# Kernel tuning notes

Measured on AMD Instinct MI355X. Metric: run time of the kernel, lower is better.

Reference implementation:

```python
import jax, jax.numpy as jnp
import numpy as np

N, K, M = 4096, 128, 512  # conformers, dihedrals, atoms


def setup_inputs() -> dict:
    key = jax.random.key(0)
    k1, k2 = jax.random.split(key)
    inp = jax.random.normal(k1, (N, K), dtype=jnp.float32)          # target dihedral deltas (rad)
    pos0 = jax.random.normal(k2, (N, M, 3), dtype=jnp.float32)      # initial conformer coordinates
    base = jnp.arange(K, dtype=jnp.int32)
    # chain molecule: dihedral k defined by atoms (k, k+1, k+2, k+3)
    angles = jnp.stack([base, base + 1, base + 2, base + 3], axis=1)  # (K, 4)
    # rdkit toBeMovedIdxList on a chain for bond (k+1, k+2): atoms k+3 .. M-1 move
    move_mask = jnp.arange(M)[None, :] > (base + 2)[:, None]          # (K, M) bool
    return {"input": inp, "pos0": pos0, "angles": angles, "move_mask": move_mask}


def _rot_matrix(theta, axis):
    # rdkit Transform3D::SetRotation: R = (1-cos)*aa^T + [[c,-sZ,sY],[sZ,c,-sX],[-sY,sX,c]]
    cosT = jnp.cos(theta)
    sinT = jnp.sin(theta)
    t = 1.0 - cosT
    outer = t[:, None, None] * axis[:, :, None] * axis[:, None, :]   # (N,3,3)
    X, Y, Z = axis[:, 0], axis[:, 1], axis[:, 2]
    mat1 = jnp.stack(
        [cosT, -sinT * Z, sinT * Y,
         sinT * Z, cosT, -sinT * X,
         -sinT * Y, sinT * X, cosT], axis=1
    ).reshape(-1, 3, 3)
    return outer + mat1


def _step(pos, x):
    ang, mask, theta = x                       # (4,), (M,), (N,)
    p = jnp.take(pos, ang, axis=1)             # (N,4,3) gather of i,j,k,l atoms
    rIJ = p[:, 1] - p[:, 0]
    rJK = p[:, 2] - p[:, 1]
    rKL = p[:, 3] - p[:, 2]
    nIJK = jnp.cross(rIJ, rJK)
    nJKL = jnp.cross(rJK, rKL)
    m = jnp.cross(nIJK, rJK)
    nrm = lambda v: jnp.linalg.norm(v, axis=-1)
    sin_arg = jnp.sum(m * nJKL, axis=-1) / (nrm(nJKL) * nrm(m))
    cos_arg = jnp.sum(nIJK * nJKL, axis=-1) / (nrm(nIJK) * nrm(nJKL))
    values = theta + jnp.arctan2(sin_arg, cos_arg)   # rotation angle per conformer
    begin = p[:, 1]                                   # rotation axis origin (atom j)
    d = p[:, 2] - p[:, 1]
    # torch.nn.functional.normalize with eps=1e-12
    axis = d / jnp.maximum(jnp.linalg.norm(d, axis=-1, keepdims=True), 1e-12)
    R = _rot_matrix(values, axis)                     # (N,3,3)
    rotated = jnp.einsum('nij,nmj->nmi', R, pos - begin[:, None, :]) + begin[:, None, :]
    pos = jnp.where(mask[None, :, None], rotated, pos)
    return pos, None


def reference(input, pos0, angles, move_mask):
    xs = (angles, move_mask, input.T)                 # scan over K dihedrals (sequential recurrence)
    pos, _ = jax.lax.scan(_step, pos0, xs)
    return pos
```

## Files before the change

### kernel.cpp

```cpp
#include <hip/hip_runtime.h>


#define NK 128
#define NM 512
#define NMOL 4096
#define TPB 256
#define WPB 4
#define MPWAVE 2

struct Aff { float qw, qx, qy, qz, tx, ty, tz; };

__device__ __forceinline__ void qrot(float qw, float qx, float qy, float qz,
                                     float vx, float vy, float vz,
                                     float& ox, float& oy, float& oz) {
    const float ux = qy*vz - qz*vy + qw*vx;
    const float uy = qz*vx - qx*vz + qw*vy;
    const float uz = qx*vy - qy*vx + qw*vz;
    ox = vx + 2.f*(qy*uz - qz*uy);
    oy = vy + 2.f*(qz*ux - qx*uz);
    oz = vz + 2.f*(qx*uy - qy*ux);
}

__device__ __forceinline__ Aff aff_compose(const Aff& Q, const Aff& P) {
    Aff r;
    r.qw = Q.qw*P.qw - Q.qx*P.qx - Q.qy*P.qy - Q.qz*P.qz;
    r.qx = Q.qw*P.qx + Q.qx*P.qw + Q.qy*P.qz - Q.qz*P.qy;
    r.qy = Q.qw*P.qy - Q.qx*P.qz + Q.qy*P.qw + Q.qz*P.qx;
    r.qz = Q.qw*P.qz + Q.qx*P.qy - Q.qy*P.qx + Q.qz*P.qw;
    float rx, ry, rz;
    qrot(Q.qw, Q.qx, Q.qy, Q.qz, P.tx, P.ty, P.tz, rx, ry, rz);
    r.tx = rx + Q.tx; r.ty = ry + Q.ty; r.tz = rz + Q.tz;
    return r;
}

__device__ __forceinline__ void qnorm(Aff& a) {
    const float r = rsqrtf(a.qw*a.qw + a.qx*a.qx + a.qy*a.qy + a.qz*a.qz);
    a.qw *= r; a.qx *= r; a.qy *= r; a.qz *= r;
}

__device__ __forceinline__ Aff build_step(const float* a, float th) {
    const float ijx=a[3]-a[0], ijy=a[4]-a[1],  ijz=a[5]-a[2];
    const float jkx=a[6]-a[3], jky=a[7]-a[4],  jkz=a[8]-a[5];
    const float klx=a[9]-a[6], kly=a[10]-a[7], klz=a[11]-a[8];
    const float n1x=ijy*jkz-ijz*jky, n1y=ijz*jkx-ijx*jkz, n1z=ijx*jky-ijy*jkx;
    const float n2x=jky*klz-jkz*kly, n2y=jkz*klx-jkx*klz, n2z=jkx*kly-jky*klx;
    const float L1=n1x*n1x+n1y*n1y+n1z*n1z;
    const float L2=n2x*n2x+n2y*n2y+n2z*n2z;
    const float dnn=n1x*n2x+n1y*n2y+n1z*n2z;
    const float cxx=n2y*n1z-n2z*n1y, cxy=n2z*n1x-n2x*n1z, cxz=n2x*n1y-n2y*n1x;
    const float g  = cxx*jkx + cxy*jky + cxz*jkz;
    const float Ljk = jkx*jkx+jky*jky+jkz*jkz;
    const float ira = rsqrtf(fmaxf(Ljk, 1e-24f));
    const float r12 = rsqrtf(fmaxf(L1*L2, 1e-30f));
    const float cphi = dnn*r12;
    const float sphi = g*r12*ira;
    const float sth = __sinf(th), cth = __cosf(th);
    const float c = cth*cphi - sth*sphi;
    const float s = sth*cphi + cth*sphi;
    const float hc = sqrtf(fmaxf(0.f, 0.5f*(1.f + c)));
    const float hs = copysignf(sqrtf(fmaxf(0.f, 0.5f*(1.f - c))), s);
    const float hsa = hs*ira;
    Aff b;
    b.qw = hc; b.qx = jkx*hsa; b.qy = jky*hsa; b.qz = jkz*hsa;
    float rx, ry, rz;
    qrot(b.qw, b.qx, b.qy, b.qz, a[3], a[4], a[5], rx, ry, rz);
    b.tx = a[3]-rx; b.ty = a[4]-ry; b.tz = a[5]-rz;
    return b;
}

#define SHFL_AFF_UP(D, S, off)                                           \
    D.qw = __shfl_up(S.qw, off, 64); D.qx = __shfl_up(S.qx, off, 64);    \
    D.qy = __shfl_up(S.qy, off, 64); D.qz = __shfl_up(S.qz, off, 64);    \
    D.tx = __shfl_up(S.tx, off, 64); D.ty = __shfl_up(S.ty, off, 64);    \
    D.tz = __shfl_up(S.tz, off, 64);

__device__ __forceinline__ void do_molecule(
    const int lane, float* __restrict__ sA, float* __restrict__ sO,
    float4* __restrict__ ob4, const float2 th2,
    const float4 Ta0, const float4 Ta1, const float4 Ta2,
    const float4 Tb0, const float4 Tb1, const float4 Tb2, const bool hasB)
{
    float A[16];
    const float2* ap2 = (const float2*)&sA[lane * 6];
    #pragma unroll
    for (int i = 0; i < 7; ++i) { const float2 v = ap2[i]; A[2*i] = v.x; A[2*i+1] = v.y; }
    A[14] = sA[lane * 6 + 14];

    Aff Bev = build_step(&A[0], th2.x);
    Aff Bod = build_step(&A[3], th2.y);
    Aff S   = aff_compose(Bev, Bod);

    #pragma unroll
    for (int off = 1; off < 64; off <<= 1) {
        Aff Q; SHFL_AFF_UP(Q, S, off);
        if (lane >= off) S = aff_compose(Q, S);
    }
    Aff E; SHFL_AFF_UP(E, S, 1);
    if (lane == 0) { E.qw = 1.f; E.qx = E.qy = E.qz = 0.f; E.tx = E.ty = E.tz = 0.f; }
    Aff Pe = aff_compose(E, Bev);
    qnorm(Pe); qnorm(S);

    {
        float ox, oy, oz;
        float* op = &sO[lane * 6 + 9];
        qrot(Pe.qw, Pe.qx, Pe.qy, Pe.qz, A[9], A[10], A[11], ox, oy, oz);
        op[0] = ox + Pe.tx; op[1] = oy + Pe.ty; op[2] = oz + Pe.tz;
        qrot(S.qw, S.qx, S.qy, S.qz, A[12], A[13], A[14], ox, oy, oz);
        op[3] = ox + S.tx;  op[4] = oy + S.ty;  op[5] = oz + S.tz;
    }
    if (lane < 9) sO[lane] = sA[lane];
    if (lane == 63) {
        float ox, oy, oz;
        qrot(S.qw, S.qx, S.qy, S.qz, sA[393], sA[394], sA[395], ox, oy, oz);
        sO[393] = ox + S.tx; sO[394] = oy + S.ty; sO[395] = oz + S.tz;
    }

    Aff F;
    F.qw = __shfl(S.qw, 63, 64); F.qx = __shfl(S.qx, 63, 64);
    F.qy = __shfl(S.qy, 63, 64); F.qz = __shfl(S.qz, 63, 64);
    F.tx = __shfl(S.tx, 63, 64); F.ty = __shfl(S.ty, 63, 64);
    F.tz = __shfl(S.tz, 63, 64);
    const float f00 = 1.f - 2.f*(F.qy*F.qy + F.qz*F.qz);
    const float f01 = 2.f*(F.qx*F.qy - F.qw*F.qz);
    const float f02 = 2.f*(F.qx*F.qz + F.qw*F.qy);
    const float f10 = 2.f*(F.qx*F.qy + F.qw*F.qz);
    const float f11 = 1.f - 2.f*(F.qx*F.qx + F.qz*F.qz);
    const float f12 = 2.f*(F.qy*F.qz - F.qw*F.qx);
    const float f20 = 2.f*(F.qx*F.qz - F.qw*F.qy);
    const float f21 = 2.f*(F.qy*F.qz + F.qw*F.qx);
    const float f22 = 1.f - 2.f*(F.qx*F.qx + F.qy*F.qy);

    const float4* sO4 = (const float4*)sO;
    ob4[lane] = sO4[lane];
    if (lane < 35) ob4[64 + lane] = sO4[64 + lane];

    #define TAIL_EMIT(b, va, vb, vc)                                          \
    do {                                                                      \
        const float x0=va.x, y0=va.y, z0=va.z;                                \
        const float x1=va.w, y1=vb.x, z1=vb.y;                                \
        const float x2=vb.z, y2=vb.w, z2=vc.x;                                \
        const float x3=vc.y, y3=vc.z, z3=vc.w;                                \
        float4 o0, o1, o2;                                                    \
        o0.x = f00*x0+f01*y0+f02*z0+F.tx; o0.y = f10*x0+f11*y0+f12*z0+F.ty;   \
        o0.z = f20*x0+f21*y0+f22*z0+F.tz; o0.w = f00*x1+f01*y1+f02*z1+F.tx;   \
        o1.x = f10*x1+f11*y1+f12*z1+F.ty; o1.y = f20*x1+f21*y1+f22*z1+F.tz;   \
        o1.z = f00*x2+f01*y2+f02*z2+F.tx; o1.w = f10*x2+f11*y2+f12*z2+F.ty;   \
        o2.x = f20*x2+f21*y2+f22*z2+F.tz; o2.y = f00*x3+f01*y3+f02*z3+F.tx;   \
        o2.z = f10*x3+f11*y3+f12*z3+F.ty; o2.w = f20*x3+f21*y3+f22*z3+F.tz;   \
        ob4[(b)] = o0; ob4[(b)+1] = o1; ob4[(b)+2] = o2;                      \
    } while (0)

    TAIL_EMIT(99 + 3*lane, Ta0, Ta1, Ta2);
    if (hasB) TAIL_EMIT(99 + 3*(64 + lane), Tb0, Tb1, Tb2);
    #undef TAIL_EMIT
}

__global__ __launch_bounds__(TPB, 2) void dihedral_pipe2_kernel(
    const float* __restrict__ theta,
    const float* __restrict__ pos0,
    float* __restrict__ out)
{
    const int tid  = threadIdx.x;
    const int lane = tid & 63;
    const int wid  = tid >> 6;
    const int molA = blockIdx.x * (WPB * MPWAVE) + wid;
    const int molB = molA + WPB;

    const float4* __restrict__ pbA = (const float4*)(pos0 + (size_t)molA * (NM*3));
    float4*       __restrict__ obA = (float4*)(out  + (size_t)molA * (NM*3));
    const float4* __restrict__ pbB = (const float4*)(pos0 + (size_t)molB * (NM*3));
    float4*       __restrict__ obB = (float4*)(out  + (size_t)molB * (NM*3));

    __shared__ float sA[WPB][400];
    __shared__ float sO[WPB][400];

    const bool hasB2 = (lane < 31);

    float4 hA0 = pbA[lane];
    float4 hA1; if (lane < 35) hA1 = pbA[64 + lane];
    const float2 thA = ((const float2*)(theta + (size_t)molA * NK))[lane];
    float4 hB0 = pbB[lane];
    float4 hB1; if (lane < 35) hB1 = pbB[64 + lane];
    const float2 thB = ((const float2*)(theta + (size_t)molB * NK))[lane];
    float4 TaA0, TaA1, TaA2, TbA0, TbA1, TbA2;
    { const int b = 99 + 3*lane; TaA0 = pbA[b]; TaA1 = pbA[b+1]; TaA2 = pbA[b+2]; }
    if (hasB2) { const int b = 99 + 3*(64 + lane); TbA0 = pbA[b]; TbA1 = pbA[b+1]; TbA2 = pbA[b+2]; }

    float4* sA4 = (float4*)sA[wid];
    sA4[lane] = hA0;
    if (lane < 35) sA4[64 + lane] = hA1;
    do_molecule(lane, sA[wid], sO[wid], obA, thA, TaA0, TaA1, TaA2, TbA0, TbA1, TbA2, hasB2);

    float4 TaB0, TaB1, TaB2, TbB0, TbB1, TbB2;
    { const int b = 99 + 3*lane; TaB0 = pbB[b]; TaB1 = pbB[b+1]; TaB2 = pbB[b+2]; }
    if (hasB2) { const int b = 99 + 3*(64 + lane); TbB0 = pbB[b]; TbB1 = pbB[b+1]; TbB2 = pbB[b+2]; }

    sA4[lane] = hB0;
    if (lane < 35) sA4[64 + lane] = hB1;
    do_molecule(lane, sA[wid], sO[wid], obB, thB, TaB0, TaB1, TaB2, TbB0, TbB1, TbB2, hasB2);
}

extern "C" void kernel_launch(void* const* d_in, const int* in_sizes, int n_in,
                              void* d_out, int out_size, void* d_ws, size_t ws_size,
                              hipStream_t stream) {
    const float* theta = (const float*)d_in[0];
    const float* pos0  = (const float*)d_in[1];
    float* out = (float*)d_out;
    dihedral_pipe2_kernel<<<NMOL / (WPB * MPWAVE), TPB, 0, stream>>>(theta, pos0, out);
}
```

Measured before the change: 18.96 us.

## Interleave two molecules per wave for ILP in the shuffle scan

Each wave now processes two adjacent molecules at once rather than one after the other, interleaving their build steps, shuffle-based prefix scans and output writes. The goal is to hide shuffle and ALU latency of the serial 6-step scan through independent instruction streams. It also drops the quaternion renormalization and doubles shared memory per wave, which adds register pressure and may reduce occupancy. The molecule-to-wave mapping changes to adjacent molecules.

```diff
diff --git a/kernel.cpp b/kernel.cpp
--- a/kernel.cpp
+++ b/kernel.cpp
@@ -6,7 +6,7 @@
 #define NMOL 4096
 #define TPB 256
 #define WPB 4
-#define MPWAVE 2
+#define MPW 2
 
 struct Aff { float qw, qx, qy, qz, tx, ty, tz; };
 
@@ -31,11 +31,6 @@
     qrot(Q.qw, Q.qx, Q.qy, Q.qz, P.tx, P.ty, P.tz, rx, ry, rz);
     r.tx = rx + Q.tx; r.ty = ry + Q.ty; r.tz = rz + Q.tz;
     return r;
-}
-
-__device__ __forceinline__ void qnorm(Aff& a) {
-    const float r = rsqrtf(a.qw*a.qw + a.qx*a.qx + a.qy*a.qy + a.qz*a.qz);
-    a.qw *= r; a.qx *= r; a.qy *= r; a.qz *= r;
 }
 
 __device__ __forceinline__ Aff build_step(const float* a, float th) {
@@ -74,88 +69,7 @@
     D.tx = __shfl_up(S.tx, off, 64); D.ty = __shfl_up(S.ty, off, 64);    \
     D.tz = __shfl_up(S.tz, off, 64);
 
-__device__ __forceinline__ void do_molecule(
-    const int lane, float* __restrict__ sA, float* __restrict__ sO,
-    float4* __restrict__ ob4, const float2 th2,
-    const float4 Ta0, const float4 Ta1, const float4 Ta2,
-    const float4 Tb0, const float4 Tb1, const float4 Tb2, const bool hasB)
-{
-    float A[16];
-    const float2* ap2 = (const float2*)&sA[lane * 6];
-    #pragma unroll
-    for (int i = 0; i < 7; ++i) { const float2 v = ap2[i]; A[2*i] = v.x; A[2*i+1] = v.y; }
-    A[14] = sA[lane * 6 + 14];
-
-    Aff Bev = build_step(&A[0], th2.x);
-    Aff Bod = build_step(&A[3], th2.y);
-    Aff S   = aff_compose(Bev, Bod);
-
-    #pragma unroll
-    for (int off = 1; off < 64; off <<= 1) {
-        Aff Q; SHFL_AFF_UP(Q, S, off);
-        if (lane >= off) S = aff_compose(Q, S);
-    }
-    Aff E; SHFL_AFF_UP(E, S, 1);
-    if (lane == 0) { E.qw = 1.f; E.qx = E.qy = E.qz = 0.f; E.tx = E.ty = E.tz = 0.f; }
-    Aff Pe = aff_compose(E, Bev);
-    qnorm(Pe); qnorm(S);
-
-    {
-        float ox, oy, oz;
-        float* op = &sO[lane * 6 + 9];
-        qrot(Pe.qw, Pe.qx, Pe.qy, Pe.qz, A[9], A[10], A[11], ox, oy, oz);
-        op[0] = ox + Pe.tx; op[1] = oy + Pe.ty; op[2] = oz + Pe.tz;
-        qrot(S.qw, S.qx, S.qy, S.qz, A[12], A[13], A[14], ox, oy, oz);
-        op[3] = ox + S.tx;  op[4] = oy + S.ty;  op[5] = oz + S.tz;
-    }
-    if (lane < 9) sO[lane] = sA[lane];
-    if (lane == 63) {
-        float ox, oy, oz;
-        qrot(S.qw, S.qx, S.qy, S.qz, sA[393], sA[394], sA[395], ox, oy, oz);
-        sO[393] = ox + S.tx; sO[394] = oy + S.ty; sO[395] = oz + S.tz;
-    }
-
-    Aff F;
-    F.qw = __shfl(S.qw, 63, 64); F.qx = __shfl(S.qx, 63, 64);
-    F.qy = __shfl(S.qy, 63, 64); F.qz = __shfl(S.qz, 63, 64);
-    F.tx = __shfl(S.tx, 63, 64); F.ty = __shfl(S.ty, 63, 64);
-    F.tz = __shfl(S.tz, 63, 64);
-    const float f00 = 1.f - 2.f*(F.qy*F.qy + F.qz*F.qz);
-    const float f01 = 2.f*(F.qx*F.qy - F.qw*F.qz);
-    const float f02 = 2.f*(F.qx*F.qz + F.qw*F.qy);
-    const float f10 = 2.f*(F.qx*F.qy + F.qw*F.qz);
-    const float f11 = 1.f - 2.f*(F.qx*F.qx + F.qz*F.qz);
-    const float f12 = 2.f*(F.qy*F.qz - F.qw*F.qx);
-    const float f20 = 2.f*(F.qx*F.qz - F.qw*F.qy);
-    const float f21 = 2.f*(F.qy*F.qz + F.qw*F.qx);
-    const float f22 = 1.f - 2.f*(F.qx*F.qx + F.qy*F.qy);
-
-    const float4* sO4 = (const float4*)sO;
-    ob4[lane] = sO4[lane];
-    if (lane < 35) ob4[64 + lane] = sO4[64 + lane];
-
-    #define TAIL_EMIT(b, va, vb, vc)                                          \
-    do {                                                                      \
-        const float x0=va.x, y0=va.y, z0=va.z;                                \
-        const float x1=va.w, y1=vb.x, z1=vb.y;                                \
-        const float x2=vb.z, y2=vb.w, z2=vc.x;                                \
-        const float x3=vc.y, y3=vc.z, z3=vc.w;                                \
-        float4 o0, o1, o2;                                                    \
-        o0.x = f00*x0+f01*y0+f02*z0+F.tx; o0.y = f10*x0+f11*y0+f12*z0+F.ty;   \
-        o0.z = f20*x0+f21*y0+f22*z0+F.tz; o0.w = f00*x1+f01*y1+f02*z1+F.tx;   \
-        o1.x = f10*x1+f11*y1+f12*z1+F.ty; o1.y = f20*x1+f21*y1+f22*z1+F.tz;   \
-        o1.z = f00*x2+f01*y2+f02*z2+F.tx; o1.w = f10*x2+f11*y2+f12*z2+F.ty;   \
-        o2.x = f20*x2+f21*y2+f22*z2+F.tz; o2.y = f00*x3+f01*y3+f02*z3+F.tx;   \
-        o2.z = f10*x3+f11*y3+f12*z3+F.ty; o2.w = f20*x3+f21*y3+f22*z3+F.tz;   \
-        ob4[(b)] = o0; ob4[(b)+1] = o1; ob4[(b)+2] = o2;                      \
-    } while (0)
-
-    TAIL_EMIT(99 + 3*lane, Ta0, Ta1, Ta2);
-    if (hasB) TAIL_EMIT(99 + 3*(64 + lane), Tb0, Tb1, Tb2);
-    #undef TAIL_EMIT
-}
-
-__global__ __launch_bounds__(TPB, 2) void dihedral_pipe2_kernel(
+__global__ __launch_bounds__(TPB, 2) void dihedral_ilp2_kernel(
     const float* __restrict__ theta,
     const float* __restrict__ pos0,
     float* __restrict__ out)
@@ -163,41 +77,148 @@
     const int tid  = threadIdx.x;
     const int lane = tid & 63;
     const int wid  = tid >> 6;
-    const int molA = blockIdx.x * (WPB * MPWAVE) + wid;
-    const int molB = molA + WPB;
+    const int molA = (blockIdx.x * WPB + wid) * MPW;
+    const int molB = molA + 1;
 
     const float4* __restrict__ pbA = (const float4*)(pos0 + (size_t)molA * (NM*3));
     float4*       __restrict__ obA = (float4*)(out  + (size_t)molA * (NM*3));
     const float4* __restrict__ pbB = (const float4*)(pos0 + (size_t)molB * (NM*3));
     float4*       __restrict__ obB = (float4*)(out  + (size_t)molB * (NM*3));
 
-    __shared__ float sA[WPB][400];
-    __shared__ float sO[WPB][400];
-
-    const bool hasB2 = (lane < 31);
+    __shared__ float sA[WPB][MPW][400];
+    __shared__ float sO[WPB][MPW][400];
+
+    const bool ex   = (lane < 35);
+    const bool has2 = (lane < 31);
 
     float4 hA0 = pbA[lane];
-    float4 hA1; if (lane < 35) hA1 = pbA[64 + lane];
+    float4 hA1; if (ex) hA1 = pbA[64 + lane];
+    float4 hB0 = pbB[lane];
+    float4 hB1; if (ex) hB1 = pbB[64 + lane];
     const float2 thA = ((const float2*)(theta + (size_t)molA * NK))[lane];
-    float4 hB0 = pbB[lane];
-    float4 hB1; if (lane < 35) hB1 = pbB[64 + lane];
     const float2 thB = ((const float2*)(theta + (size_t)molB * NK))[lane];
-    float4 TaA0, TaA1, TaA2, TbA0, TbA1, TbA2;
-    { const int b = 99 + 3*lane; TaA0 = pbA[b]; TaA1 = pbA[b+1]; TaA2 = pbA[b+2]; }
-    if (hasB2) { const int b = 99 + 3*(64 + lane); TbA0 = pbA[b]; TbA1 = pbA[b+1]; TbA2 = pbA[b+2]; }
-
-    float4* sA4 = (float4*)sA[wid];
-    sA4[lane] = hA0;
-    if (lane < 35) sA4[64 + lane] = hA1;
-    do_molecule(lane, sA[wid], sO[wid], obA, thA, TaA0, TaA1, TaA2, TbA0, TbA1, TbA2, hasB2);
-
-    float4 TaB0, TaB1, TaB2, TbB0, TbB1, TbB2;
-    { const int b = 99 + 3*lane; TaB0 = pbB[b]; TaB1 = pbB[b+1]; TaB2 = pbB[b+2]; }
-    if (hasB2) { const int b = 99 + 3*(64 + lane); TbB0 = pbB[b]; TbB1 = pbB[b+1]; TbB2 = pbB[b+2]; }
-
-    sA4[lane] = hB0;
-    if (lane < 35) sA4[64 + lane] = hB1;
-    do_molecule(lane, sA[wid], sO[wid], obB, thB, TaB0, TaB1, TaB2, TbB0, TbB1, TbB2, hasB2);
+    float4 TA0, TA1, TA2, TA3, TA4, TA5;
+    { const int b = 99 + 3*lane; TA0 = pbA[b]; TA1 = pbA[b+1]; TA2 = pbA[b+2]; }
+    if (has2) { const int b = 99 + 3*(64 + lane); TA3 = pbA[b]; TA4 = pbA[b+1]; TA5 = pbA[b+2]; }
+
+    float4* sA4A = (float4*)sA[wid][0];
+    float4* sA4B = (float4*)sA[wid][1];
+    sA4A[lane] = hA0; if (ex) sA4A[64 + lane] = hA1;
+    sA4B[lane] = hB0; if (ex) sA4B[64 + lane] = hB1;
+
+    float AA[16], AB[16];
+    {
+        const float2* a2 = (const float2*)&sA[wid][0][lane * 6];
+        const float2* b2 = (const float2*)&sA[wid][1][lane * 6];
+        #pragma unroll
+        for (int i = 0; i < 7; ++i) {
+            const float2 va = a2[i]; AA[2*i] = va.x; AA[2*i+1] = va.y;
+            const float2 vb = b2[i]; AB[2*i] = vb.x; AB[2*i+1] = vb.y;
+        }
+        AA[14] = sA[wid][0][lane * 6 + 14];
+        AB[14] = sA[wid][1][lane * 6 + 14];
+    }
+
+    Aff BevA = build_step(&AA[0], thA.x);
+    Aff BevB = build_step(&AB[0], thB.x);
+    Aff BodA = build_step(&AA[3], thA.y);
+    Aff BodB = build_step(&AB[3], thB.y);
+    Aff SA_ = aff_compose(BevA, BodA);
+    Aff SB_ = aff_compose(BevB, BodB);
+
+    #pragma unroll
+    for (int off = 1; off < 64; off <<= 1) {
+        Aff QA; SHFL_AFF_UP(QA, SA_, off);
+        Aff QB; SHFL_AFF_UP(QB, SB_, off);
+        if (lane >= off) SA_ = aff_compose(QA, SA_);
+        if (lane >= off) SB_ = aff_compose(QB, SB_);
+    }
+    Aff EA; SHFL_AFF_UP(EA, SA_, 1);
+    Aff EB; SHFL_AFF_UP(EB, SB_, 1);
+    if (lane == 0) {
+        EA.qw = 1.f; EA.qx = EA.qy = EA.qz = 0.f; EA.tx = EA.ty = EA.tz = 0.f;
+        EB.qw = 1.f; EB.qx = EB.qy = EB.qz = 0.f; EB.tx = EB.ty = EB.tz = 0.f;
+    }
+    Aff PeA = aff_compose(EA, BevA);
+    Aff PeB = aff_compose(EB, BevB);
+
+    float4 TB0, TB1, TB2, TB3, TB4, TB5;
+    { const int b = 99 + 3*lane; TB0 = pbB[b]; TB1 = pbB[b+1]; TB2 = pbB[b+2]; }
+    if (has2) { const int b = 99 + 3*(64 + lane); TB3 = pbB[b]; TB4 = pbB[b+1]; TB5 = pbB[b+2]; }
+
+    {
+        float ox, oy, oz;
+        float* opA = &sO[wid][0][lane * 6 + 9];
+        qrot(PeA.qw, PeA.qx, PeA.qy, PeA.qz, AA[9], AA[10], AA[11], ox, oy, oz);
+        opA[0] = ox + PeA.tx; opA[1] = oy + PeA.ty; opA[2] = oz + PeA.tz;
+        qrot(SA_.qw, SA_.qx, SA_.qy, SA_.qz, AA[12], AA[13], AA[14], ox, oy, oz);
+        opA[3] = ox + SA_.tx; opA[4] = oy + SA_.ty; opA[5] = oz + SA_.tz;
+        float* opB = &sO[wid][1][lane * 6 + 9];
+        qrot(PeB.qw, PeB.qx, PeB.qy, PeB.qz, AB[9], AB[10], AB[11], ox, oy, oz);
+        opB[0] = ox + PeB.tx; opB[1] = oy + PeB.ty; opB[2] = oz + PeB.tz;
+        qrot(SB_.qw, SB_.qx, SB_.qy, SB_.qz, AB[12], AB[13], AB[14], ox, oy, oz);
+        opB[3] = ox + SB_.tx; opB[4] = oy + SB_.ty; opB[5] = oz + SB_.tz;
+    }
+    if (lane < 9) { sO[wid][0][lane] = sA[wid][0][lane]; sO[wid][1][lane] = sA[wid][1][lane]; }
+    if (lane == 63) {
+        float ox, oy, oz;
+        qrot(SA_.qw, SA_.qx, SA_.qy, SA_.qz, sA[wid][0][393], sA[wid][0][394], sA[wid][0][395], ox, oy, oz);
+        sO[wid][0][393] = ox + SA_.tx; sO[wid][0][394] = oy + SA_.ty; sO[wid][0][395] = oz + SA_.tz;
+        qrot(SB_.qw, SB_.qx, SB_.qy, SB_.qz, sA[wid][1][393], sA[wid][1][394], sA[wid][1][395], ox, oy, oz);
+        sO[wid][1][393] = ox + SB_.tx; sO[wid][1][394] = oy + SB_.ty; sO[wid][1][395] = oz + SB_.tz;
+    }
+
+    Aff FA, FB;
+    FA.qw = __shfl(SA_.qw, 63, 64); FA.qx = __shfl(SA_.qx, 63, 64);
+    FA.qy = __shfl(SA_.qy, 63, 64); FA.qz = __shfl(SA_.qz, 63, 64);
+    FA.tx = __shfl(SA_.tx, 63, 64); FA.ty = __shfl(SA_.ty, 63, 64);
+    FA.tz = __shfl(SA_.tz, 63, 64);
+    FB.qw = __shfl(SB_.qw, 63, 64); FB.qx = __shfl(SB_.qx, 63, 64);
+    FB.qy = __shfl(SB_.qy, 63, 64); FB.qz = __shfl(SB_.qz, 63, 64);
+    FB.tx = __shfl(SB_.tx, 63, 64); FB.ty = __shfl(SB_.ty, 63, 64);
+    FB.tz = __shfl(SB_.tz, 63, 64);
+
+    #define MAT_OF(F, f00,f01,f02,f10,f11,f12,f20,f21,f22)                   \
+        const float f00 = 1.f - 2.f*(F.qy*F.qy + F.qz*F.qz);                 \
+        const float f01 = 2.f*(F.qx*F.qy - F.qw*F.qz);                       \
+        const float f02 = 2.f*(F.qx*F.qz + F.qw*F.qy);                       \
+        const float f10 = 2.f*(F.qx*F.qy + F.qw*F.qz);                       \
+        const float f11 = 1.f - 2.f*(F.qx*F.qx + F.qz*F.qz);                 \
+        const float f12 = 2.f*(F.qy*F.qz - F.qw*F.qx);                       \
+        const float f20 = 2.f*(F.qx*F.qz - F.qw*F.qy);                       \
+        const float f21 = 2.f*(F.qy*F.qz + F.qw*F.qx);                       \
+        const float f22 = 1.f - 2.f*(F.qx*F.qx + F.qy*F.qy);
+    MAT_OF(FA, a00,a01,a02,a10,a11,a12,a20,a21,a22)
+    MAT_OF(FB, b00,b01,b02,b10,b11,b12,b20,b21,b22)
+    #undef MAT_OF
+
+    #define TAIL_EMIT(ob4, b, va, vb, vc, f00,f01,f02,f10,f11,f12,f20,f21,f22, FT) \
+    do {                                                                      \
+        const float x0=va.x, y0=va.y, z0=va.z;                                \
+        const float x1=va.w, y1=vb.x, z1=vb.y;                                \
+        const float x2=vb.z, y2=vb.w, z2=vc.x;                                \
+        const float x3=vc.y, y3=vc.z, z3=vc.w;                                \
+        float4 o0, o1, o2;                                                    \
+        o0.x = f00*x0+f01*y0+f02*z0+FT.tx; o0.y = f10*x0+f11*y0+f12*z0+FT.ty; \
+        o0.z = f20*x0+f21*y0+f22*z0+FT.tz; o0.w = f00*x1+f01*y1+f02*z1+FT.tx; \
+        o1.x = f10*x1+f11*y1+f12*z1+FT.ty; o1.y = f20*x1+f21*y1+f22*z1+FT.tz; \
+        o1.z = f00*x2+f01*y2+f02*z2+FT.tx; o1.w = f10*x2+f11*y2+f12*z2+FT.ty; \
+        o2.x = f20*x2+f21*y2+f22*z2+FT.tz; o2.y = f00*x3+f01*y3+f02*z3+FT.tx; \
+        o2.z = f10*x3+f11*y3+f12*z3+FT.ty; o2.w = f20*x3+f21*y3+f22*z3+FT.tz; \
+        ob4[(b)] = o0; ob4[(b)+1] = o1; ob4[(b)+2] = o2;                      \
+    } while (0)
+
+    TAIL_EMIT(obA, 99 + 3*lane, TA0, TA1, TA2, a00,a01,a02,a10,a11,a12,a20,a21,a22, FA);
+    if (has2) TAIL_EMIT(obA, 99 + 3*(64 + lane), TA3, TA4, TA5, a00,a01,a02,a10,a11,a12,a20,a21,a22, FA);
+
+    const float4* sO4A = (const float4*)sO[wid][0];
+    const float4* sO4B = (const float4*)sO[wid][1];
+    obA[lane] = sO4A[lane]; if (ex) obA[64 + lane] = sO4A[64 + lane];
+    obB[lane] = sO4B[lane]; if (ex) obB[64 + lane] = sO4B[64 + lane];
+
+    TAIL_EMIT(obB, 99 + 3*lane, TB0, TB1, TB2, b00,b01,b02,b10,b11,b12,b20,b21,b22, FB);
+    if (has2) TAIL_EMIT(obB, 99 + 3*(64 + lane), TB3, TB4, TB5, b00,b01,b02,b10,b11,b12,b20,b21,b22, FB);
+    #undef TAIL_EMIT
 }
 
 extern "C" void kernel_launch(void* const* d_in, const int* in_sizes, int n_in,
@@ -206,5 +227,5 @@
     const float* theta = (const float*)d_in[0];
     const float* pos0  = (const float*)d_in[1];
     float* out = (float*)d_out;
-    dihedral_pipe2_kernel<<<NMOL / (WPB * MPWAVE), TPB, 0, stream>>>(theta, pos0, out);
-}
+    dihedral_ilp2_kernel<<<NMOL / (WPB * MPW), TPB, 0, stream>>>(theta, pos0, out);
+}
```

Result: no change. 18.99 us (+0.1%).
